# Performance work log

Measured on AMD Instinct MI355X. Metric: run time of the kernel, lower is better.

## Reference

```python
import jax, jax.numpy as jnp
import numpy as np

B, P, CIN = 512, 64, 512       # batch, h*w feature positions, resnet18 channels
HID, EMB, NCLS, T = 512, 512, 96, 30


def setup_inputs() -> dict:
    key = jax.random.key(0)
    ks = jax.random.split(key, 16)
    s = 0.02
    return {
        "features": jax.random.normal(ks[0], (B, P, CIN), jnp.float32),
        "targets": jax.random.randint(ks[1], (B, T), 0, NCLS),
        "max_length": T,
        "Wfc": jax.random.normal(ks[2], (HID, CIN), jnp.float32) * s,
        "bfc": jnp.zeros((HID,), jnp.float32),
        "emb_table": jax.random.normal(ks[3], (NCLS, EMB), jnp.float32) * s,
        "Wa": jax.random.normal(ks[4], (HID, HID + EMB), jnp.float32) * s,
        "ba": jnp.zeros((HID,), jnp.float32),
        "Wc": jax.random.normal(ks[5], (HID, HID + EMB), jnp.float32) * s,
        "bc": jnp.zeros((HID,), jnp.float32),
        "Wih": jax.random.normal(ks[6], (4 * HID, HID), jnp.float32) * s,
        "Whh": jax.random.normal(ks[7], (4 * HID, HID), jnp.float32) * s,
        "bih": jnp.zeros((4 * HID,), jnp.float32),
        "bhh": jnp.zeros((4 * HID,), jnp.float32),
        "Wo": jax.random.normal(ks[8], (NCLS, HID), jnp.float32) * s,
        "bo": jnp.zeros((NCLS,), jnp.float32),
    }


def reference(features, targets, max_length, Wfc, bfc, emb_table, Wa, ba,
              Wc, bc, Wih, Whh, bih, bhh, Wo, bo):
    b = features.shape[0]
    hid = Wfc.shape[0]
    feats = features @ Wfc.T + bfc                       # [b, P, hid]
    # teacher forcing: input at t=0 is token 0, then targets[:, t-1]
    in_ids = jnp.concatenate(
        [jnp.zeros((b, 1), targets.dtype), targets[:, : max_length - 1]], axis=1)
    emb_seq = emb_table[in_ids].transpose(1, 0, 2)       # [T, b, emb]

    def step(carry, emb):
        h, c = carry
        # first softmax is over the hidden dim (as in the original module)
        a = jax.nn.softmax(jnp.concatenate([h, emb], -1) @ Wa.T + ba, axis=-1)  # [b,hid]
        scores = jnp.einsum('bph,bh->bp', feats, a)      # [b, P]
        w = jax.nn.softmax(scores, axis=-1)
        ctx = jnp.einsum('bp,bph->bh', w, feats)         # [b, hid]
        x = jnp.concatenate([emb, ctx], -1) @ Wc.T + bc  # [b, hid]
        gates = x @ Wih.T + bih + h @ Whh.T + bhh        # [b, 4*hid]
        i, f, g, o = jnp.split(gates, 4, axis=-1)        # torch gate order i,f,g,o
        c_new = jax.nn.sigmoid(f) * c + jax.nn.sigmoid(i) * jnp.tanh(g)
        h_new = jax.nn.sigmoid(o) * jnp.tanh(c_new)
        out = h_new @ Wo.T + bo                          # [b, ncls]
        return (h_new, c_new), out

    h0 = jnp.zeros((b, hid), feats.dtype)
    (_, _), outs = jax.lax.scan(step, (h0, h0), emb_seq)
    return outs.transpose(1, 0, 2)                       # [b, T, ncls]
```

## Files before the change

### kernel.cpp

```cpp
#include <hip/hip_runtime.h>
#include <math.h>

static constexpr int BATCH = 512;
static constexpr int PPOS  = 64;
static constexpr int HIDC  = 512;

typedef __attribute__((ext_vector_type(8))) short bf8;
typedef __attribute__((ext_vector_type(4))) float f4;

static __device__ __forceinline__ float sigmoidf_(float x) { return 1.f / (1.f + expf(-x)); }

static __device__ __forceinline__ short f2bf(float x) {
  unsigned u = __float_as_uint(x);
  u = u + 0x7FFF + ((u >> 16) & 1);
  return (short)(u >> 16);
}
static __device__ __forceinline__ float bf2f(short s) {
  return __uint_as_float(((unsigned)(unsigned short)s) << 16);
}

__global__ void transpose_k(const float* __restrict__ src, float* __restrict__ dst, int R, int C, int ld) {
  __shared__ float tile[32][33];
  int c0 = blockIdx.x * 32, r0 = blockIdx.y * 32;
  int x = threadIdx.x;
  for (int yy = threadIdx.y; yy < 32; yy += 8) {
    int r = r0 + yy, c = c0 + x;
    if (r < R && c < C) tile[yy][x] = src[(size_t)r * ld + c];
  }
  __syncthreads();
  for (int yy = threadIdx.y; yy < 32; yy += 8) {
    int c = c0 + yy, r = r0 + x;
    if (r < R && c < C) dst[(size_t)c * R + r] = tile[x][yy];
  }
}

__global__ void bfuse_k(const float* __restrict__ Wih, const float* __restrict__ bc,
                        const float* __restrict__ bih, const float* __restrict__ bhh,
                        float* __restrict__ bf) {
  int n = blockIdx.x * 256 + threadIdx.x;
  float s = bih[n] + bhh[n];
  const float* w = Wih + (size_t)n * 512;
  for (int m = 0; m < 512; m++) s += w[m] * bc[m];
  bf[n] = s;
}

__global__ void build_btg_k(const float* __restrict__ tmp, const float* __restrict__ Whh,
                            short* __restrict__ hi, short* __restrict__ lo) {
  int idx = blockIdx.x * 256 + threadIdx.x;
  int cp = idx >> 10, k = idx & 1023;
  int j = cp >> 2, g = cp & 3;
  int n = g * 512 + j;
  float v = (k < 512) ? tmp[(size_t)(512 + k) * 2048 + n] : Whh[(size_t)n * 512 + (k - 512)];
  short h = f2bf(v);
  hi[idx] = h;
  lo[idx] = f2bf(v - bf2f(h));
}

__global__ void split_k(const float* __restrict__ src, short* __restrict__ hi, short* __restrict__ lo, int n) {
  int i = blockIdx.x * 256 + threadIdx.x;
  if (i < n) {
    float x = src[i];
    short h = f2bf(x);
    hi[i] = h;
    lo[i] = f2bf(x - bf2f(h));
  }
}

__global__ void split_wah_k(const float* __restrict__ Wa, short* __restrict__ hi, short* __restrict__ lo) {
  int idx = blockIdx.x * 256 + threadIdx.x;
  int n = idx >> 9, k = idx & 511;
  float v = Wa[(size_t)n * 1024 + k];
  short h = f2bf(v);
  hi[idx] = h;
  lo[idx] = f2bf(v - bf2f(h));
}

__global__ __launch_bounds__(256) void gemb_k(const float* __restrict__ emb_table, const float* __restrict__ tmp,
                                              const float* __restrict__ bfused, float* __restrict__ Gemb_p) {
  __shared__ float emb_s[4][512];
  int tid = threadIdx.x;
  int n0 = blockIdx.x * 256;
  int e0 = blockIdx.y * 4;
  for (int i = tid; i < 2048; i += 256)
    emb_s[i >> 9][i & 511] = emb_table[(size_t)(e0 + (i >> 9)) * 512 + (i & 511)];
  __syncthreads();
  int n = n0 + tid;
  float acc[4] = {};
  for (int k = 0; k < 512; k++) {
    float w = tmp[(size_t)k * 2048 + n];
#pragma unroll
    for (int e = 0; e < 4; e++) acc[e] += emb_s[e][k] * w;
  }
  int cp = (n & 511) * 4 + (n >> 9);
  float b = bfused[n];
#pragma unroll
  for (int e = 0; e < 4; e++) Gemb_p[(size_t)(e0 + e) * 2048 + cp] = acc[e] + b;
}

__global__ __launch_bounds__(256) void za_k(const float* __restrict__ emb_table, const float* __restrict__ WaT_emb,
                                            const float* __restrict__ ba, float* __restrict__ Za) {
  __shared__ float emb_s[4][512];
  int tid = threadIdx.x;
  int n0 = blockIdx.x * 256;
  int e0 = blockIdx.y * 4;
  for (int i = tid; i < 2048; i += 256)
    emb_s[i >> 9][i & 511] = emb_table[(size_t)(e0 + (i >> 9)) * 512 + (i & 511)];
  __syncthreads();
  int n = n0 + tid;
  float acc[4] = {};
  for (int k = 0; k < 512; k++) {
    float w = WaT_emb[(size_t)k * 512 + n];
#pragma unroll
    for (int e = 0; e < 4; e++) acc[e] += emb_s[e][k] * w;
  }
  float b = ba[n];
#pragma unroll
  for (int e = 0; e < 4; e++) Za[(size_t)(e0 + e) * 512 + n] = acc[e] + b;
}

__global__ __launch_bounds__(256) void feats_mfma_k(const float* __restrict__ A,
                                                    const short* __restrict__ BTh, const short* __restrict__ BTl,
                                                    const float* __restrict__ bias, float* __restrict__ C) {
  __shared__ short Ah[2][64][40], Al[2][64][40], Bh[2][128][40], Bl[2][128][40];
  int blk = blockIdx.x;
  int xt = (blk >> 3) & 3;
  int ytile = (blk >> 5) * 8 + (blk & 7);
  int row0 = ytile * 64, col0 = xt * 128;
  int tid = threadIdx.x;
  int lane = tid & 63, wave = tid >> 6;
  int wm = (wave & 1) * 32, wn = (wave >> 1) * 64;
  int r15 = lane & 15, q8 = (lane >> 4) * 8;
  int smA = tid >> 2, skA = (tid & 3) * 8;
  int smB = tid >> 1, skB = (tid & 1) * 16;
  const float* Ap = A + (size_t)(row0 + smA) * 512 + skA;
  const short* Bhp = BTh + (size_t)(col0 + smB) * 512 + skB;
  const short* Blp = BTl + (size_t)(col0 + smB) * 512 + skB;
  float4 a0 = *(const float4*)Ap, a1 = *(const float4*)(Ap + 4);
  bf8 bh0 = *(const bf8*)Bhp, bh1 = *(const bf8*)(Bhp + 8);
  bf8 bl0 = *(const bf8*)Blp, bl1 = *(const bf8*)(Blp + 8);
  f4 acc[2][4] = {};
  for (int kt = 0; kt < 16; kt++) {
    int buf = kt & 1;
    {
      float av[8] = {a0.x, a0.y, a0.z, a0.w, a1.x, a1.y, a1.z, a1.w};
      bf8 ahv, alv;
#pragma unroll
      for (int i = 0; i < 8; i++) {
        short h = f2bf(av[i]);
        ahv[i] = h;
        alv[i] = f2bf(av[i] - bf2f(h));
      }
      *(bf8*)&Ah[buf][smA][skA] = ahv;
      *(bf8*)&Al[buf][smA][skA] = alv;
      *(bf8*)&Bh[buf][smB][skB] = bh0;
      *(bf8*)&Bh[buf][smB][skB + 8] = bh1;
      *(bf8*)&Bl[buf][smB][skB] = bl0;
      *(bf8*)&Bl[buf][smB][skB + 8] = bl1;
    }
    if (kt + 1 < 16) {
      Ap += 32; Bhp += 32; Blp += 32;
      a0 = *(const float4*)Ap; a1 = *(const float4*)(Ap + 4);
      bh0 = *(const bf8*)Bhp; bh1 = *(const bf8*)(Bhp + 8);
      bl0 = *(const bf8*)Blp; bl1 = *(const bf8*)(Blp + 8);
    }
    __syncthreads();
    bf8 fah[2], fal[2], fbh[4], fbl[4];
#pragma unroll
    for (int r = 0; r < 2; r++) {
      fah[r] = *(const bf8*)&Ah[buf][wm + r * 16 + r15][q8];
      fal[r] = *(const bf8*)&Al[buf][wm + r * 16 + r15][q8];
    }
#pragma unroll
    for (int c = 0; c < 4; c++) {
      fbh[c] = *(const bf8*)&Bh[buf][wn + c * 16 + r15][q8];
      fbl[c] = *(const bf8*)&Bl[buf][wn + c * 16 + r15][q8];
    }
#pragma unroll
    for (int r = 0; r < 2; r++)
#pragma unroll
      for (int c = 0; c < 4; c++) {
        acc[r][c] = __builtin_amdgcn_mfma_f32_16x16x32_bf16(fah[r], fbh[c], acc[r][c], 0, 0, 0);
        acc[r][c] = __builtin_amdgcn_mfma_f32_16x16x32_bf16(fal[r], fbh[c], acc[r][c], 0, 0, 0);
        acc[r][c] = __builtin_amdgcn_mfma_f32_16x16x32_bf16(fah[r], fbl[c], acc[r][c], 0, 0, 0);
      }
  }
#pragma unroll
  for (int r = 0; r < 2; r++)
#pragma unroll
    for (int c = 0; c < 4; c++) {
      int col = col0 + wn + c * 16 + r15;
      float bv = bias[col];
#pragma unroll
      for (int i = 0; i < 4; i++) {
        int row = row0 + wm + r * 16 + (lane >> 4) * 4 + i;
        C[(size_t)row * 512 + col] = acc[r][c][i] + bv;
      }
    }
}

__global__ __launch_bounds__(256) void tmp_mfma_k(const float* __restrict__ A,
                                                  const short* __restrict__ BTh, const short* __restrict__ BTl,
                                                  float* __restrict__ C) {
  __shared__ short Ah[2][64][40], Al[2][64][40], Bh[2][128][40], Bl[2][128][40];
  int row0 = blockIdx.y * 64, col0 = blockIdx.x * 128;
  int tid = threadIdx.x;
  int lane = tid & 63, wave = tid >> 6;
  int wm = (wave & 1) * 32, wn = (wave >> 1) * 64;
  int r15 = lane & 15, q8 = (lane >> 4) * 8;
  int smA = tid >> 2, skA = (tid & 3) * 8;
  int smB = tid >> 1, skB = (tid & 1) * 16;
  const float* Ap = A + (size_t)(row0 + smA) * 512 + skA;
  const short* Bhp = BTh + (size_t)(col0 + smB) * 512 + skB;
  const short* Blp = BTl + (size_t)(col0 + smB) * 512 + skB;
  float4 a0 = *(const float4*)Ap, a1 = *(const float4*)(Ap + 4);
  bf8 bh0 = *(const bf8*)Bhp, bh1 = *(const bf8*)(Bhp + 8);
  bf8 bl0 = *(const bf8*)Blp, bl1 = *(const bf8*)(Blp + 8);
  f4 acc[2][4] = {};
  for (int kt = 0; kt < 16; kt++) {
    int buf = kt & 1;
    {
      float av[8] = {a0.x, a0.y, a0.z, a0.w, a1.x, a1.y, a1.z, a1.w};
      bf8 ahv, alv;
#pragma unroll
      for (int i = 0; i < 8; i++) {
        short h = f2bf(av[i]);
        ahv[i] = h;
        alv[i] = f2bf(av[i] - bf2f(h));
      }
      *(bf8*)&Ah[buf][smA][skA] = ahv;
      *(bf8*)&Al[buf][smA][skA] = alv;
      *(bf8*)&Bh[buf][smB][skB] = bh0;
      *(bf8*)&Bh[buf][smB][skB + 8] = bh1;
      *(bf8*)&Bl[buf][smB][skB] = bl0;
      *(bf8*)&Bl[buf][smB][skB + 8] = bl1;
    }
    if (kt + 1 < 16) {
      Ap += 32; Bhp += 32; Blp += 32;
      a0 = *(const float4*)Ap; a1 = *(const float4*)(Ap + 4);
      bh0 = *(const bf8*)Bhp; bh1 = *(const bf8*)(Bhp + 8);
      bl0 = *(const bf8*)Blp; bl1 = *(const bf8*)(Blp + 8);
    }
    __syncthreads();
    bf8 fah[2], fal[2], fbh[4], fbl[4];
#pragma unroll
    for (int r = 0; r < 2; r++) {
      fah[r] = *(const bf8*)&Ah[buf][wm + r * 16 + r15][q8];
      fal[r] = *(const bf8*)&Al[buf][wm + r * 16 + r15][q8];
    }
#pragma unroll
    for (int c = 0; c < 4; c++) {
      fbh[c] = *(const bf8*)&Bh[buf][wn + c * 16 + r15][q8];
      fbl[c] = *(const bf8*)&Bl[buf][wn + c * 16 + r15][q8];
    }
#pragma unroll
    for (int r = 0; r < 2; r++)
#pragma unroll
      for (int c = 0; c < 4; c++) {
        acc[r][c] = __builtin_amdgcn_mfma_f32_16x16x32_bf16(fah[r], fbh[c], acc[r][c], 0, 0, 0);
        acc[r][c] = __builtin_amdgcn_mfma_f32_16x16x32_bf16(fal[r], fbh[c], acc[r][c], 0, 0, 0);
        acc[r][c] = __builtin_amdgcn_mfma_f32_16x16x32_bf16(fah[r], fbl[c], acc[r][c], 0, 0, 0);
      }
  }
#pragma unroll
  for (int r = 0; r < 2; r++)
#pragma unroll
    for (int c = 0; c < 4; c++) {
      int col = col0 + wn + c * 16 + r15;
#pragma unroll
      for (int i = 0; i < 4; i++) {
        int row = row0 + wm + r * 16 + (lane >> 4) * 4 + i;
        C[(size_t)row * 2048 + col] = acc[r][c][i];
      }
    }
}

__global__ __launch_bounds__(256) void z_mfma_k(const short* __restrict__ h_hi, const short* __restrict__ h_lo,
                                                const short* __restrict__ BTh, const short* __restrict__ BTl,
                                                float* __restrict__ zbuf) {
  __shared__ short Ah[2][32][72], Al[2][32][72], Bh[2][32][72], Bl[2][32][72];
  int tid = threadIdx.x;
  int lane = tid & 63, wave = tid >> 6;
  int wm = (wave & 1) * 16, wn = (wave >> 1) * 16;
  int r15 = lane & 15, q4 = (lane >> 4) * 4, q8 = (lane >> 4) * 8;
  int row0 = blockIdx.y * 32, col0 = blockIdx.x * 32;
  int kz = blockIdx.z * 256;
  int sm = tid >> 3, sk = (tid & 7) * 8;
  const short* ahp = h_hi + (size_t)(row0 + sm) * 512 + kz + sk;
  const short* alp = h_lo + (size_t)(row0 + sm) * 512 + kz + sk;
  const short* bhp = BTh + (size_t)(col0 + sm) * 512 + kz + sk;
  const short* blp = BTl + (size_t)(col0 + sm) * 512 + kz + sk;
  bf8 ah = *(const bf8*)ahp, al = *(const bf8*)alp;
  bf8 bh = *(const bf8*)bhp, bl = *(const bf8*)blp;
  f4 acc = {};
  for (int kt = 0; kt < 4; kt++) {
    int buf = kt & 1;
    *(bf8*)&Ah[buf][sm][sk] = ah;
    *(bf8*)&Al[buf][sm][sk] = al;
    *(bf8*)&Bh[buf][sm][sk] = bh;
    *(bf8*)&Bl[buf][sm][sk] = bl;
    if (kt + 1 < 4) {
      ahp += 64; alp += 64; bhp += 64; blp += 64;
      ah = *(const bf8*)ahp; al = *(const bf8*)alp;
      bh = *(const bf8*)bhp; bl = *(const bf8*)blp;
    }
    __syncthreads();
#pragma unroll
    for (int ks = 0; ks < 2; ks++) {
      bf8 fah = *(const bf8*)&Ah[buf][wm + r15][ks * 32 + q8];
      bf8 fal = *(const bf8*)&Al[buf][wm + r15][ks * 32 + q8];
      bf8 fbh = *(const bf8*)&Bh[buf][wn + r15][ks * 32 + q8];
      bf8 fbl = *(const bf8*)&Bl[buf][wn + r15][ks * 32 + q8];
      acc = __builtin_amdgcn_mfma_f32_16x16x32_bf16(fah, fbh, acc, 0, 0, 0);
      acc = __builtin_amdgcn_mfma_f32_16x16x32_bf16(fal, fbh, acc, 0, 0, 0);
      acc = __builtin_amdgcn_mfma_f32_16x16x32_bf16(fah, fbl, acc, 0, 0, 0);
    }
  }
  float* zo = zbuf + (size_t)blockIdx.z * (512 * 512);
  int col = col0 + wn + r15;
#pragma unroll
  for (int i = 0; i < 4; i++)
    zo[(size_t)(row0 + wm + q4 + i) * 512 + col] = acc[i];
}

__global__ __launch_bounds__(512) void attn_fin_k(const float* __restrict__ zbuf,
                                                  const int* __restrict__ targets, int t, int T,
                                                  const float* __restrict__ Za, const float* __restrict__ feats,
                                                  short* __restrict__ ctx_hi, short* __restrict__ ctx_lo) {
  __shared__ float a_s[512];
  __shared__ float redm[8], reds[8];
  __shared__ float sc_s[64];
  __shared__ float w_s[64];
  __shared__ float cpart[8][512];
  int tid = threadIdx.x;
  int wid = tid >> 6, lane = tid & 63;
  int b = blockIdx.x;
  int id = (t == 0) ? 0 : targets[b * T + t - 1];

  const float4* fbase = (const float4*)(feats + (size_t)b * PPOS * 512);
  float4 f1[8], f2[8];
#pragma unroll
  for (int q = 0; q < 8; q++) {
    int p = wid * 8 + q;
    f1[q] = fbase[(size_t)p * 128 + lane];
    f2[q] = fbase[(size_t)p * 128 + 64 + lane];
  }

  float zv = zbuf[(size_t)b * 512 + tid] + zbuf[(size_t)(512 * 512) + b * 512 + tid]
           + Za[(size_t)id * 512 + tid];
  float m = zv;
#pragma unroll
  for (int off = 32; off; off >>= 1) m = fmaxf(m, __shfl_xor(m, off, 64));
  if (lane == 0) redm[wid] = m;
  __syncthreads();
  float M = redm[0];
#pragma unroll
  for (int w = 1; w < 8; w++) M = fmaxf(M, redm[w]);
  float e = expf(zv - M);
  float s = e;
#pragma unroll
  for (int off = 32; off; off >>= 1) s += __shfl_xor(s, off, 64);
  if (lane == 0) reds[wid] = s;
  __syncthreads();
  float S = 0.f;
#pragma unroll
  for (int w = 0; w < 8; w++) S += reds[w];
  a_s[tid] = e * (1.f / S);
  __syncthreads();

  float4 a1 = ((const float4*)a_s)[lane];
  float4 a2 = ((const float4*)a_s)[lane + 64];
#pragma unroll
  for (int q = 0; q < 8; q++) {
    float d = f1[q].x * a1.x + f1[q].y * a1.y + f1[q].z * a1.z + f1[q].w * a1.w
            + f2[q].x * a2.x + f2[q].y * a2.y + f2[q].z * a2.z + f2[q].w * a2.w;
#pragma unroll
    for (int off = 32; off; off >>= 1) d += __shfl_xor(d, off, 64);
    if (lane == 0) sc_s[wid * 8 + q] = d;
  }
  __syncthreads();

  if (wid == 0) {
    float v = sc_s[lane];
    float mm = v;
#pragma unroll
    for (int off = 32; off; off >>= 1) mm = fmaxf(mm, __shfl_xor(mm, off, 64));
    float ee = expf(v - mm);
    float ss = ee;
#pragma unroll
    for (int off = 32; off; off >>= 1) ss += __shfl_xor(ss, off, 64);
    w_s[lane] = ee / ss;
  }
  __syncthreads();

  float4 c1 = {0.f, 0.f, 0.f, 0.f}, c2 = {0.f, 0.f, 0.f, 0.f};
#pragma unroll
  for (int q = 0; q < 8; q++) {
    float wp = w_s[wid * 8 + q];
    c1.x += wp * f1[q].x; c1.y += wp * f1[q].y; c1.z += wp * f1[q].z; c1.w += wp * f1[q].w;
    c2.x += wp * f2[q].x; c2.y += wp * f2[q].y; c2.z += wp * f2[q].z; c2.w += wp * f2[q].w;
  }
  ((float4*)&cpart[wid][0])[lane] = c1;
  ((float4*)&cpart[wid][256])[lane] = c2;
  __syncthreads();

  float acc = 0.f;
#pragma unroll
  for (int w = 0; w < 8; w++) acc += cpart[w][tid];
  short hh = f2bf(acc);
  ctx_hi[(size_t)b * 512 + tid] = hh;
  ctx_lo[(size_t)b * 512 + tid] = f2bf(acc - bf2f(hh));
}

__global__ __launch_bounds__(256) void gates_mfma_k(const short* __restrict__ ctx_hi, const short* __restrict__ ctx_lo,
                                                    const short* __restrict__ h_hi_in, const short* __restrict__ h_lo_in,
                                                    const int* __restrict__ targets, int t, int T,
                                                    const short* __restrict__ BTh, const short* __restrict__ BTl,
                                                    const float* __restrict__ Gemb_p,
                                                    float* __restrict__ cbuf, float* __restrict__ h_new,
                                                    short* __restrict__ h_hi_out, short* __restrict__ h_lo_out) {
  __shared__ short Ah[2][32][72], Al[2][32][72], Bh[2][64][72], Bl[2][64][72];
  __shared__ float Cs[32][68];
  int tid = threadIdx.x;
  int lane = tid & 63, wave = tid >> 6;
  int wn = wave * 16;
  int r15 = lane & 15, q8 = (lane >> 4) * 8;
  int row0 = blockIdx.y * 32, col0 = blockIdx.x * 64;
  int smA = tid >> 3, skA = (tid & 7) * 8;
  int smB = tid >> 2, skB = (tid & 3) * 16;
  const short* actx_h = ctx_hi + (size_t)(row0 + smA) * 512;
  const short* actx_l = ctx_lo + (size_t)(row0 + smA) * 512;
  const short* ahst_h = h_hi_in + (size_t)(row0 + smA) * 512;
  const short* ahst_l = h_lo_in + (size_t)(row0 + smA) * 512;
  const short* Bhp = BTh + (size_t)(col0 + smB) * 1024 + skB;
  const short* Blp = BTl + (size_t)(col0 + smB) * 1024 + skB;
  bf8 ah = *(const bf8*)(actx_h + skA), al = *(const bf8*)(actx_l + skA);
  bf8 bh0 = *(const bf8*)Bhp, bh1 = *(const bf8*)(Bhp + 8);
  bf8 bl0 = *(const bf8*)Blp, bl1 = *(const bf8*)(Blp + 8);
  f4 acc[2] = {};
  for (int kt = 0; kt < 16; kt++) {
    int buf = kt & 1;
    *(bf8*)&Ah[buf][smA][skA] = ah;
    *(bf8*)&Al[buf][smA][skA] = al;
    *(bf8*)&Bh[buf][smB][skB] = bh0;
    *(bf8*)&Bh[buf][smB][skB + 8] = bh1;
    *(bf8*)&Bl[buf][smB][skB] = bl0;
    *(bf8*)&Bl[buf][smB][skB + 8] = bl1;
    if (kt + 1 < 16) {
      int kk = (kt + 1) * 64 + skA;
      if (kk < 512) {
        ah = *(const bf8*)(actx_h + kk);
        al = *(const bf8*)(actx_l + kk);
      } else {
        ah = *(const bf8*)(ahst_h + kk - 512);
        al = *(const bf8*)(ahst_l + kk - 512);
      }
      Bhp += 64; Blp += 64;
      bh0 = *(const bf8*)Bhp; bh1 = *(const bf8*)(Bhp + 8);
      bl0 = *(const bf8*)Blp; bl1 = *(const bf8*)(Blp + 8);
    }
    __syncthreads();
#pragma unroll
    for (int ks = 0; ks < 2; ks++) {
      bf8 fah[2], fal[2];
#pragma unroll
      for (int r = 0; r < 2; r++) {
        fah[r] = *(const bf8*)&Ah[buf][r * 16 + r15][ks * 32 + q8];
        fal[r] = *(const bf8*)&Al[buf][r * 16 + r15][ks * 32 + q8];
      }
      bf8 fbh = *(const bf8*)&Bh[buf][wn + r15][ks * 32 + q8];
      bf8 fbl = *(const bf8*)&Bl[buf][wn + r15][ks * 32 + q8];
#pragma unroll
      for (int r = 0; r < 2; r++) {
        acc[r] = __builtin_amdgcn_mfma_f32_16x16x32_bf16(fah[r], fbh, acc[r], 0, 0, 0);
        acc[r] = __builtin_amdgcn_mfma_f32_16x16x32_bf16(fal[r], fbh, acc[r], 0, 0, 0);
        acc[r] = __builtin_amdgcn_mfma_f32_16x16x32_bf16(fah[r], fbl, acc[r], 0, 0, 0);
      }
    }
  }
#pragma unroll
  for (int r = 0; r < 2; r++)
#pragma unroll
    for (int i = 0; i < 4; i++)
      Cs[r * 16 + (lane >> 4) * 4 + i][wn + r15] = acc[r][i];
  __syncthreads();
#pragma unroll
  for (int it = 0; it < 2; it++) {
    int idx = it * 256 + tid;
    int row = idx >> 4, jj = idx & 15;
    int b = row0 + row;
    int jg = (col0 >> 2) + jj;
    int id = (t == 0) ? 0 : targets[b * T + t - 1];
    float4 g4 = *(const float4*)(Gemb_p + (size_t)id * 2048 + col0 + jj * 4);
    float ig = sigmoidf_(Cs[row][jj * 4 + 0] + g4.x);
    float fg = sigmoidf_(Cs[row][jj * 4 + 1] + g4.y);
    float gg = tanhf(Cs[row][jj * 4 + 2] + g4.z);
    float og = sigmoidf_(Cs[row][jj * 4 + 3] + g4.w);
    float cn = fg * cbuf[(size_t)b * 512 + jg] + ig * gg;
    float hn = og * tanhf(cn);
    cbuf[(size_t)b * 512 + jg] = cn;
    h_new[(size_t)b * 512 + jg] = hn;
    short hh = f2bf(hn);
    h_hi_out[(size_t)b * 512 + jg] = hh;
    h_lo_out[(size_t)b * 512 + jg] = f2bf(hn - bf2f(hh));
  }
}

__global__ __launch_bounds__(256) void out_gemm_k(const float* __restrict__ h_hist, const float* __restrict__ WoT,
                                                  const float* __restrict__ bo, float* __restrict__ out, int T) {
  __shared__ float As[16][68];
  __shared__ float Bs[16][96];
  int tid = threadIdx.x;
  int tx = tid & 15, ty = tid >> 4;
  int row0 = blockIdx.x * 64;
  float acc[4][6] = {};
  for (int k0 = 0; k0 < 512; k0 += 16) {
    {
      int r = tid >> 2;
      int kk = (tid & 3) * 4;
      float4 v = *(const float4*)(h_hist + (size_t)(row0 + r) * 512 + k0 + kk);
      As[kk + 0][r] = v.x; As[kk + 1][r] = v.y; As[kk + 2][r] = v.z; As[kk + 3][r] = v.w;
    }
#pragma unroll
    for (int i = 0; i < 6; i++) {
      int e = tid + 256 * i;
      int kb = e / 96, n = e - kb * 96;
      Bs[kb][n] = WoT[(size_t)(k0 + kb) * 96 + n];
    }
    __syncthreads();
#pragma unroll
    for (int q = 0; q < 16; q++) {
      float av[4], bvv[6];
#pragma unroll
      for (int i = 0; i < 4; i++) av[i] = As[q][ty * 4 + i];
#pragma unroll
      for (int j = 0; j < 6; j++) bvv[j] = Bs[q][tx * 6 + j];
#pragma unroll
      for (int i = 0; i < 4; i++)
#pragma unroll
        for (int j = 0; j < 6; j++) acc[i][j] += av[i] * bvv[j];
    }
    __syncthreads();
  }
#pragma unroll
  for (int i = 0; i < 4; i++)
#pragma unroll
    for (int j = 0; j < 6; j++) {
      int row = row0 + ty * 4 + i;
      int tt = row >> 9, bb = row & 511;
      int cc = tx * 6 + j;
      out[((size_t)bb * T + tt) * 96 + cc] = acc[i][j] + bo[cc];
    }
}

extern "C" void kernel_launch(void* const* d_in, const int* in_sizes, int n_in,
                              void* d_out, int out_size, void* d_ws, size_t ws_size,
                              hipStream_t stream) {
  const float* features  = (const float*)d_in[0];
  const int*   targets   = (const int*)d_in[1];
  const float* Wfc       = (const float*)d_in[3];
  const float* bfc       = (const float*)d_in[4];
  const float* emb_table = (const float*)d_in[5];
  const float* Wa        = (const float*)d_in[6];
  const float* ba        = (const float*)d_in[7];
  const float* Wc        = (const float*)d_in[8];
  const float* bc        = (const float*)d_in[9];
  const float* Wih       = (const float*)d_in[10];
  const float* Whh       = (const float*)d_in[11];
  const float* bih       = (const float*)d_in[12];
  const float* bhh       = (const float*)d_in[13];
  const float* Wo        = (const float*)d_in[14];
  const float* bo        = (const float*)d_in[15];
  float* out = (float*)d_out;
  int T = in_sizes[1] / BATCH;

  char* base = (char*)d_ws;
  auto alloc = [&](size_t bytes) -> char* {
    char* p = base;
    base += (bytes + 255) & ~(size_t)255;
    return p;
  };
  float* feats   = (float*)alloc((size_t)BATCH * PPOS * HIDC * 4);
  float* WaT_emb = (float*)alloc(512 * 512 * 4);
  float* WcT     = (float*)alloc(1024 * 512 * 4);
  float* tmp     = (float*)alloc((size_t)1024 * 2048 * 4);
  short* Wih_hi  = (short*)alloc((size_t)2048 * 512 * 2);
  short* Wih_lo  = (short*)alloc((size_t)2048 * 512 * 2);
  short* BTg_hi  = (short*)alloc((size_t)2048 * 1024 * 2);
  short* BTg_lo  = (short*)alloc((size_t)2048 * 1024 * 2);
  short* Wfc_hi  = (short*)alloc(512 * 512 * 2);
  short* Wfc_lo  = (short*)alloc(512 * 512 * 2);
  short* WaH_hi  = (short*)alloc(512 * 512 * 2);
  short* WaH_lo  = (short*)alloc(512 * 512 * 2);
  float* Gemb_p  = (float*)alloc(96 * 2048 * 4);
  float* Za      = (float*)alloc(96 * 512 * 4);
  float* bfused  = (float*)alloc(2048 * 4);
  float* WoT     = (float*)alloc(512 * 96 * 4);
  float* cbuf    = (float*)alloc(BATCH * HIDC * 4);
  float* zbuf    = (float*)alloc((size_t)2 * BATCH * HIDC * 4);
  short* ctx_hi  = (short*)alloc(BATCH * HIDC * 2);
  short* ctx_lo  = (short*)alloc(BATCH * HIDC * 2);
  short* h_hi    = (short*)alloc(BATCH * HIDC * 2);
  short* h_lo    = (short*)alloc(BATCH * HIDC * 2);
  float* h_hist  = (float*)alloc((size_t)T * BATCH * HIDC * 4);

  dim3 tb(32, 8);
  transpose_k<<<dim3(16, 16), tb, 0, stream>>>(Wa + 512, WaT_emb, 512, 512, 1024);
  transpose_k<<<dim3(32, 16), tb, 0, stream>>>(Wc, WcT, 512, 1024, 1024);
  transpose_k<<<dim3(16, 3),  tb, 0, stream>>>(Wo, WoT, 96, 512, 512);

  split_k<<<(2048 * 512) / 256, 256, 0, stream>>>(Wih, Wih_hi, Wih_lo, 2048 * 512);
  split_k<<<(512 * 512) / 256, 256, 0, stream>>>(Wfc, Wfc_hi, Wfc_lo, 512 * 512);
  split_wah_k<<<(512 * 512) / 256, 256, 0, stream>>>(Wa, WaH_hi, WaH_lo);

  tmp_mfma_k<<<dim3(16, 16), 256, 0, stream>>>(WcT, Wih_hi, Wih_lo, tmp);

  bfuse_k<<<8, 256, 0, stream>>>(Wih, bc, bih, bhh, bfused);
  build_btg_k<<<(2048 * 1024) / 256, 256, 0, stream>>>(tmp, Whh, BTg_hi, BTg_lo);
  gemb_k<<<dim3(8, 24), 256, 0, stream>>>(emb_table, tmp, bfused, Gemb_p);
  za_k<<<dim3(2, 24), 256, 0, stream>>>(emb_table, WaT_emb, ba, Za);

  feats_mfma_k<<<2048, 256, 0, stream>>>(features, Wfc_hi, Wfc_lo, bfc, feats);

  hipMemsetAsync(cbuf, 0, (size_t)BATCH * HIDC * 4, stream);
  hipMemsetAsync(h_hi, 0, (size_t)BATCH * HIDC * 2, stream);
  hipMemsetAsync(h_lo, 0, (size_t)BATCH * HIDC * 2, stream);

  for (int t = 0; t < T; t++) {
    float* h_new = h_hist + (size_t)t * BATCH * HIDC;
    z_mfma_k<<<dim3(16, 16, 2), 256, 0, stream>>>(h_hi, h_lo, WaH_hi, WaH_lo, zbuf);
    attn_fin_k<<<512, 512, 0, stream>>>(zbuf, targets, t, T, Za, feats, ctx_hi, ctx_lo);
    gates_mfma_k<<<dim3(32, 16), 256, 0, stream>>>(ctx_hi, ctx_lo, h_hi, h_lo, targets, t, T,
                                                   BTg_hi, BTg_lo, Gemb_p, cbuf, h_new, h_hi, h_lo);
  }
  out_gemm_k<<<(T * BATCH) / 64, 256, 0, stream>>>(h_hist, WoT, bo, out, T);
}
```

Measured before the change: 1.445 ms.

## Pre-pack weight operands in MFMA fragment order and load B directly to registers

```diff
diff --git a/kernel.cpp b/kernel.cpp
--- a/kernel.cpp
+++ b/kernel.cpp
@@ -44,18 +44,6 @@
   bf[n] = s;
 }
 
-__global__ void build_btg_k(const float* __restrict__ tmp, const float* __restrict__ Whh,
-                            short* __restrict__ hi, short* __restrict__ lo) {
-  int idx = blockIdx.x * 256 + threadIdx.x;
-  int cp = idx >> 10, k = idx & 1023;
-  int j = cp >> 2, g = cp & 3;
-  int n = g * 512 + j;
-  float v = (k < 512) ? tmp[(size_t)(512 + k) * 2048 + n] : Whh[(size_t)n * 512 + (k - 512)];
-  short h = f2bf(v);
-  hi[idx] = h;
-  lo[idx] = f2bf(v - bf2f(h));
-}
-
 __global__ void split_k(const float* __restrict__ src, short* __restrict__ hi, short* __restrict__ lo, int n) {
   int i = blockIdx.x * 256 + threadIdx.x;
   if (i < n) {
@@ -66,10 +54,27 @@
   }
 }
 
-__global__ void split_wah_k(const float* __restrict__ Wa, short* __restrict__ hi, short* __restrict__ lo) {
+__global__ void pack_split_k(const float* __restrict__ src, int ld,
+                             short* __restrict__ hi, short* __restrict__ lo) {
   int idx = blockIdx.x * 256 + threadIdx.x;
-  int n = idx >> 9, k = idx & 511;
-  float v = Wa[(size_t)n * 1024 + k];
+  int j = idx & 7, lane = (idx >> 3) & 63, kf = (idx >> 9) & 15, cg = idx >> 13;
+  int n = cg * 16 + (lane & 15);
+  int k = kf * 32 + ((lane >> 4) << 3) + j;
+  float v = src[(size_t)n * ld + k];
+  short h = f2bf(v);
+  hi[idx] = h;
+  lo[idx] = f2bf(v - bf2f(h));
+}
+
+__global__ void build_btg_pack_k(const float* __restrict__ tmp, const float* __restrict__ Whh,
+                                 short* __restrict__ hi, short* __restrict__ lo) {
+  int idx = blockIdx.x * 256 + threadIdx.x;
+  int j = idx & 7, lane = (idx >> 3) & 63, kf = (idx >> 9) & 31, cg = idx >> 14;
+  int cp = cg * 16 + (lane & 15);
+  int k = kf * 32 + ((lane >> 4) << 3) + j;
+  int jj = cp >> 2, g = cp & 3;
+  int n = g * 512 + jj;
+  float v = (k < 512) ? tmp[(size_t)(512 + k) * 2048 + n] : Whh[(size_t)n * 512 + (k - 512)];
   short h = f2bf(v);
   hi[idx] = h;
   lo[idx] = f2bf(v - bf2f(h));
@@ -119,13 +124,91 @@
 }
 
 __global__ __launch_bounds__(256) void feats_mfma_k(const float* __restrict__ A,
-                                                    const short* __restrict__ BTh, const short* __restrict__ BTl,
+                                                    const short* __restrict__ Ph, const short* __restrict__ Pl,
                                                     const float* __restrict__ bias, float* __restrict__ C) {
-  __shared__ short Ah[2][64][40], Al[2][64][40], Bh[2][128][40], Bl[2][128][40];
+  __shared__ short Ah[2][64][40], Al[2][64][40];
   int blk = blockIdx.x;
   int xt = (blk >> 3) & 3;
   int ytile = (blk >> 5) * 8 + (blk & 7);
   int row0 = ytile * 64, col0 = xt * 128;
+  int tid = threadIdx.x;
+  int lane = tid & 63, wave = tid >> 6;
+  int wm = (wave & 1) * 32, wn = (wave >> 1) * 64;
+  int r15 = lane & 15, q8 = (lane >> 4) * 8;
+  int smA = tid >> 2, skA = (tid & 3) * 8;
+  const float* Ap = A + (size_t)(row0 + smA) * 512 + skA;
+  int cg0 = (col0 + wn) >> 4;
+  const short* pbh = Ph + (size_t)cg0 * 8192 + lane * 8;
+  const short* pbl = Pl + (size_t)cg0 * 8192 + lane * 8;
+  float4 a0 = *(const float4*)Ap, a1 = *(const float4*)(Ap + 4);
+  bf8 bhc[4], blc[4], bhn[4], bln[4];
+#pragma unroll
+  for (int c = 0; c < 4; c++) {
+    bhc[c] = *(const bf8*)(pbh + c * 8192);
+    blc[c] = *(const bf8*)(pbl + c * 8192);
+  }
+  f4 acc[2][4] = {};
+#pragma unroll 2
+  for (int kt = 0; kt < 16; kt++) {
+    int buf = kt & 1;
+    {
+      float av[8] = {a0.x, a0.y, a0.z, a0.w, a1.x, a1.y, a1.z, a1.w};
+      bf8 ahv, alv;
+#pragma unroll
+      for (int i = 0; i < 8; i++) {
+        short h = f2bf(av[i]);
+        ahv[i] = h;
+        alv[i] = f2bf(av[i] - bf2f(h));
+      }
+      *(bf8*)&Ah[buf][smA][skA] = ahv;
+      *(bf8*)&Al[buf][smA][skA] = alv;
+    }
+    if (kt + 1 < 16) {
+      Ap += 32;
+      a0 = *(const float4*)Ap; a1 = *(const float4*)(Ap + 4);
+#pragma unroll
+      for (int c = 0; c < 4; c++) {
+        bhn[c] = *(const bf8*)(pbh + c * 8192 + (kt + 1) * 512);
+        bln[c] = *(const bf8*)(pbl + c * 8192 + (kt + 1) * 512);
+      }
+    }
+    __syncthreads();
+    bf8 fah[2], fal[2];
+#pragma unroll
+    for (int r = 0; r < 2; r++) {
+      fah[r] = *(const bf8*)&Ah[buf][wm + r * 16 + r15][q8];
+      fal[r] = *(const bf8*)&Al[buf][wm + r * 16 + r15][q8];
+    }
+#pragma unroll
+    for (int r = 0; r < 2; r++)
+#pragma unroll
+      for (int c = 0; c < 4; c++) {
+        acc[r][c] = __builtin_amdgcn_mfma_f32_16x16x32_bf16(fah[r], bhc[c], acc[r][c], 0, 0, 0);
+        acc[r][c] = __builtin_amdgcn_mfma_f32_16x16x32_bf16(fal[r], bhc[c], acc[r][c], 0, 0, 0);
+        acc[r][c] = __builtin_amdgcn_mfma_f32_16x16x32_bf16(fah[r], blc[c], acc[r][c], 0, 0, 0);
+      }
+#pragma unroll
+    for (int c = 0; c < 4; c++) { bhc[c] = bhn[c]; blc[c] = bln[c]; }
+  }
+#pragma unroll
+  for (int r = 0; r < 2; r++)
+#pragma unroll
+    for (int c = 0; c < 4; c++) {
+      int col = col0 + wn + c * 16 + r15;
+      float bv = bias[col];
+#pragma unroll
+      for (int i = 0; i < 4; i++) {
+        int row = row0 + wm + r * 16 + (lane >> 4) * 4 + i;
+        C[(size_t)row * 512 + col] = acc[r][c][i] + bv;
+      }
+    }
+}
+
+__global__ __launch_bounds__(256) void tmp_mfma_k(const float* __restrict__ A,
+                                                  const short* __restrict__ BTh, const short* __restrict__ BTl,
+                                                  float* __restrict__ C) {
+  __shared__ short Ah[2][64][40], Al[2][64][40], Bh[2][128][40], Bl[2][128][40];
+  int row0 = blockIdx.y * 64, col0 = blockIdx.x * 128;
   int tid = threadIdx.x;
   int lane = tid & 63, wave = tid >> 6;
   int wm = (wave & 1) * 32, wn = (wave >> 1) * 64;
@@ -189,83 +272,6 @@
 #pragma unroll
     for (int c = 0; c < 4; c++) {
       int col = col0 + wn + c * 16 + r15;
-      float bv = bias[col];
-#pragma unroll
-      for (int i = 0; i < 4; i++) {
-        int row = row0 + wm + r * 16 + (lane >> 4) * 4 + i;
-        C[(size_t)row * 512 + col] = acc[r][c][i] + bv;
-      }
-    }
-}
-
-__global__ __launch_bounds__(256) void tmp_mfma_k(const float* __restrict__ A,
-                                                  const short* __restrict__ BTh, const short* __restrict__ BTl,
-                                                  float* __restrict__ C) {
-  __shared__ short Ah[2][64][40], Al[2][64][40], Bh[2][128][40], Bl[2][128][40];
-  int row0 = blockIdx.y * 64, col0 = blockIdx.x * 128;
-  int tid = threadIdx.x;
-  int lane = tid & 63, wave = tid >> 6;
-  int wm = (wave & 1) * 32, wn = (wave >> 1) * 64;
-  int r15 = lane & 15, q8 = (lane >> 4) * 8;
-  int smA = tid >> 2, skA = (tid & 3) * 8;
-  int smB = tid >> 1, skB = (tid & 1) * 16;
-  const float* Ap = A + (size_t)(row0 + smA) * 512 + skA;
-  const short* Bhp = BTh + (size_t)(col0 + smB) * 512 + skB;
-  const short* Blp = BTl + (size_t)(col0 + smB) * 512 + skB;
-  float4 a0 = *(const float4*)Ap, a1 = *(const float4*)(Ap + 4);
-  bf8 bh0 = *(const bf8*)Bhp, bh1 = *(const bf8*)(Bhp + 8);
-  bf8 bl0 = *(const bf8*)Blp, bl1 = *(const bf8*)(Blp + 8);
-  f4 acc[2][4] = {};
-  for (int kt = 0; kt < 16; kt++) {
-    int buf = kt & 1;
-    {
-      float av[8] = {a0.x, a0.y, a0.z, a0.w, a1.x, a1.y, a1.z, a1.w};
-      bf8 ahv, alv;
-#pragma unroll
-      for (int i = 0; i < 8; i++) {
-        short h = f2bf(av[i]);
-        ahv[i] = h;
-        alv[i] = f2bf(av[i] - bf2f(h));
-      }
-      *(bf8*)&Ah[buf][smA][skA] = ahv;
-      *(bf8*)&Al[buf][smA][skA] = alv;
-      *(bf8*)&Bh[buf][smB][skB] = bh0;
-      *(bf8*)&Bh[buf][smB][skB + 8] = bh1;
-      *(bf8*)&Bl[buf][smB][skB] = bl0;
-      *(bf8*)&Bl[buf][smB][skB + 8] = bl1;
-    }
-    if (kt + 1 < 16) {
-      Ap += 32; Bhp += 32; Blp += 32;
-      a0 = *(const float4*)Ap; a1 = *(const float4*)(Ap + 4);
-      bh0 = *(const bf8*)Bhp; bh1 = *(const bf8*)(Bhp + 8);
-      bl0 = *(const bf8*)Blp; bl1 = *(const bf8*)(Blp + 8);
-    }
-    __syncthreads();
-    bf8 fah[2], fal[2], fbh[4], fbl[4];
-#pragma unroll
-    for (int r = 0; r < 2; r++) {
-      fah[r] = *(const bf8*)&Ah[buf][wm + r * 16 + r15][q8];
-      fal[r] = *(const bf8*)&Al[buf][wm + r * 16 + r15][q8];
-    }
-#pragma unroll
-    for (int c = 0; c < 4; c++) {
-      fbh[c] = *(const bf8*)&Bh[buf][wn + c * 16 + r15][q8];
-      fbl[c] = *(const bf8*)&Bl[buf][wn + c * 16 + r15][q8];
-    }
-#pragma unroll
-    for (int r = 0; r < 2; r++)
-#pragma unroll
-      for (int c = 0; c < 4; c++) {
-        acc[r][c] = __builtin_amdgcn_mfma_f32_16x16x32_bf16(fah[r], fbh[c], acc[r][c], 0, 0, 0);
-        acc[r][c] = __builtin_amdgcn_mfma_f32_16x16x32_bf16(fal[r], fbh[c], acc[r][c], 0, 0, 0);
-        acc[r][c] = __builtin_amdgcn_mfma_f32_16x16x32_bf16(fah[r], fbl[c], acc[r][c], 0, 0, 0);
-      }
-  }
-#pragma unroll
-  for (int r = 0; r < 2; r++)
-#pragma unroll
-    for (int c = 0; c < 4; c++) {
-      int col = col0 + wn + c * 16 + r15;
 #pragma unroll
       for (int i = 0; i < 4; i++) {
         int row = row0 + wm + r * 16 + (lane >> 4) * 4 + i;
@@ -275,9 +281,9 @@
 }
 
 __global__ __launch_bounds__(256) void z_mfma_k(const short* __restrict__ h_hi, const short* __restrict__ h_lo,
-                                                const short* __restrict__ BTh, const short* __restrict__ BTl,
+                                                const short* __restrict__ Ph, const short* __restrict__ Pl,
                                                 float* __restrict__ zbuf) {
-  __shared__ short Ah[2][32][72], Al[2][32][72], Bh[2][32][72], Bl[2][32][72];
+  __shared__ short Ah[2][32][72], Al[2][32][72];
   int tid = threadIdx.x;
   int lane = tid & 63, wave = tid >> 6;
   int wm = (wave & 1) * 16, wn = (wave >> 1) * 16;
@@ -287,33 +293,42 @@
   int sm = tid >> 3, sk = (tid & 7) * 8;
   const short* ahp = h_hi + (size_t)(row0 + sm) * 512 + kz + sk;
   const short* alp = h_lo + (size_t)(row0 + sm) * 512 + kz + sk;
-  const short* bhp = BTh + (size_t)(col0 + sm) * 512 + kz + sk;
-  const short* blp = BTl + (size_t)(col0 + sm) * 512 + kz + sk;
+  int cg = (col0 + wn) >> 4;
+  const short* pbh = Ph + (size_t)cg * 8192 + (size_t)blockIdx.z * 8 * 512 + lane * 8;
+  const short* pbl = Pl + (size_t)cg * 8192 + (size_t)blockIdx.z * 8 * 512 + lane * 8;
   bf8 ah = *(const bf8*)ahp, al = *(const bf8*)alp;
-  bf8 bh = *(const bf8*)bhp, bl = *(const bf8*)blp;
+  bf8 bhc[2], blc[2], bhn[2], bln[2];
+#pragma unroll
+  for (int ks = 0; ks < 2; ks++) {
+    bhc[ks] = *(const bf8*)(pbh + ks * 512);
+    blc[ks] = *(const bf8*)(pbl + ks * 512);
+  }
   f4 acc = {};
+#pragma unroll 2
   for (int kt = 0; kt < 4; kt++) {
     int buf = kt & 1;
     *(bf8*)&Ah[buf][sm][sk] = ah;
     *(bf8*)&Al[buf][sm][sk] = al;
-    *(bf8*)&Bh[buf][sm][sk] = bh;
-    *(bf8*)&Bl[buf][sm][sk] = bl;
     if (kt + 1 < 4) {
-      ahp += 64; alp += 64; bhp += 64; blp += 64;
+      ahp += 64; alp += 64;
       ah = *(const bf8*)ahp; al = *(const bf8*)alp;
-      bh = *(const bf8*)bhp; bl = *(const bf8*)blp;
+#pragma unroll
+      for (int ks = 0; ks < 2; ks++) {
+        bhn[ks] = *(const bf8*)(pbh + ((kt + 1) * 2 + ks) * 512);
+        bln[ks] = *(const bf8*)(pbl + ((kt + 1) * 2 + ks) * 512);
+      }
     }
     __syncthreads();
 #pragma unroll
     for (int ks = 0; ks < 2; ks++) {
       bf8 fah = *(const bf8*)&Ah[buf][wm + r15][ks * 32 + q8];
       bf8 fal = *(const bf8*)&Al[buf][wm + r15][ks * 32 + q8];
-      bf8 fbh = *(const bf8*)&Bh[buf][wn + r15][ks * 32 + q8];
-      bf8 fbl = *(const bf8*)&Bl[buf][wn + r15][ks * 32 + q8];
-      acc = __builtin_amdgcn_mfma_f32_16x16x32_bf16(fah, fbh, acc, 0, 0, 0);
-      acc = __builtin_amdgcn_mfma_f32_16x16x32_bf16(fal, fbh, acc, 0, 0, 0);
-      acc = __builtin_amdgcn_mfma_f32_16x16x32_bf16(fah, fbl, acc, 0, 0, 0);
-    }
+      acc = __builtin_amdgcn_mfma_f32_16x16x32_bf16(fah, bhc[ks], acc, 0, 0, 0);
+      acc = __builtin_amdgcn_mfma_f32_16x16x32_bf16(fal, bhc[ks], acc, 0, 0, 0);
+      acc = __builtin_amdgcn_mfma_f32_16x16x32_bf16(fah, blc[ks], acc, 0, 0, 0);
+    }
+#pragma unroll
+    for (int ks = 0; ks < 2; ks++) { bhc[ks] = bhn[ks]; blc[ks] = bln[ks]; }
   }
   float* zo = zbuf + (size_t)blockIdx.z * (512 * 512);
   int col = col0 + wn + r15;
@@ -414,11 +429,11 @@
 __global__ __launch_bounds__(256) void gates_mfma_k(const short* __restrict__ ctx_hi, const short* __restrict__ ctx_lo,
                                                     const short* __restrict__ h_hi_in, const short* __restrict__ h_lo_in,
                                                     const int* __restrict__ targets, int t, int T,
-                                                    const short* __restrict__ BTh, const short* __restrict__ BTl,
+                                                    const short* __restrict__ Ph, const short* __restrict__ Pl,
                                                     const float* __restrict__ Gemb_p,
                                                     float* __restrict__ cbuf, float* __restrict__ h_new,
                                                     short* __restrict__ h_hi_out, short* __restrict__ h_lo_out) {
-  __shared__ short Ah[2][32][72], Al[2][32][72], Bh[2][64][72], Bl[2][64][72];
+  __shared__ short Ah[2][32][72], Al[2][32][72];
   __shared__ float Cs[32][68];
   int tid = threadIdx.x;
   int lane = tid & 63, wave = tid >> 6;
@@ -426,25 +441,26 @@
   int r15 = lane & 15, q8 = (lane >> 4) * 8;
   int row0 = blockIdx.y * 32, col0 = blockIdx.x * 64;
   int smA = tid >> 3, skA = (tid & 7) * 8;
-  int smB = tid >> 2, skB = (tid & 3) * 16;
   const short* actx_h = ctx_hi + (size_t)(row0 + smA) * 512;
   const short* actx_l = ctx_lo + (size_t)(row0 + smA) * 512;
   const short* ahst_h = h_hi_in + (size_t)(row0 + smA) * 512;
   const short* ahst_l = h_lo_in + (size_t)(row0 + smA) * 512;
-  const short* Bhp = BTh + (size_t)(col0 + smB) * 1024 + skB;
-  const short* Blp = BTl + (size_t)(col0 + smB) * 1024 + skB;
+  int cg = (col0 >> 4) + wave;
+  const short* pbh = Ph + (size_t)cg * 16384 + lane * 8;
+  const short* pbl = Pl + (size_t)cg * 16384 + lane * 8;
   bf8 ah = *(const bf8*)(actx_h + skA), al = *(const bf8*)(actx_l + skA);
-  bf8 bh0 = *(const bf8*)Bhp, bh1 = *(const bf8*)(Bhp + 8);
-  bf8 bl0 = *(const bf8*)Blp, bl1 = *(const bf8*)(Blp + 8);
+  bf8 bhc[2], blc[2], bhn[2], bln[2];
+#pragma unroll
+  for (int ks = 0; ks < 2; ks++) {
+    bhc[ks] = *(const bf8*)(pbh + ks * 512);
+    blc[ks] = *(const bf8*)(pbl + ks * 512);
+  }
   f4 acc[2] = {};
+#pragma unroll 2
   for (int kt = 0; kt < 16; kt++) {
     int buf = kt & 1;
     *(bf8*)&Ah[buf][smA][skA] = ah;
     *(bf8*)&Al[buf][smA][skA] = al;
-    *(bf8*)&Bh[buf][smB][skB] = bh0;
-    *(bf8*)&Bh[buf][smB][skB + 8] = bh1;
-    *(bf8*)&Bl[buf][smB][skB] = bl0;
-    *(bf8*)&Bl[buf][smB][skB + 8] = bl1;
     if (kt + 1 < 16) {
       int kk = (kt + 1) * 64 + skA;
       if (kk < 512) {
@@ -454,9 +470,11 @@
         ah = *(const bf8*)(ahst_h + kk - 512);
         al = *(const bf8*)(ahst_l + kk - 512);
       }
-      Bhp += 64; Blp += 64;
-      bh0 = *(const bf8*)Bhp; bh1 = *(const bf8*)(Bhp + 8);
-      bl0 = *(const bf8*)Blp; bl1 = *(const bf8*)(Blp + 8);
+#pragma unroll
+      for (int ks = 0; ks < 2; ks++) {
+        bhn[ks] = *(const bf8*)(pbh + ((kt + 1) * 2 + ks) * 512);
+        bln[ks] = *(const bf8*)(pbl + ((kt + 1) * 2 + ks) * 512);
+      }
     }
     __syncthreads();
 #pragma unroll
@@ -467,15 +485,15 @@
         fah[r] = *(const bf8*)&Ah[buf][r * 16 + r15][ks * 32 + q8];
         fal[r] = *(const bf8*)&Al[buf][r * 16 + r15][ks * 32 + q8];
       }
-      bf8 fbh = *(const bf8*)&Bh[buf][wn + r15][ks * 32 + q8];
-      bf8 fbl = *(const bf8*)&Bl[buf][wn + r15][ks * 32 + q8];
 #pragma unroll
       for (int r = 0; r < 2; r++) {
-        acc[r] = __builtin_amdgcn_mfma_f32_16x16x32_bf16(fah[r], fbh, acc[r], 0, 0, 0);
-        acc[r] = __builtin_amdgcn_mfma_f32_16x16x32_bf16(fal[r], fbh, acc[r], 0, 0, 0);
-        acc[r] = __builtin_amdgcn_mfma_f32_16x16x32_bf16(fah[r], fbl, acc[r], 0, 0, 0);
-      }
-    }
+        acc[r] = __builtin_amdgcn_mfma_f32_16x16x32_bf16(fah[r], bhc[ks], acc[r], 0, 0, 0);
+        acc[r] = __builtin_amdgcn_mfma_f32_16x16x32_bf16(fal[r], bhc[ks], acc[r], 0, 0, 0);
+        acc[r] = __builtin_amdgcn_mfma_f32_16x16x32_bf16(fah[r], blc[ks], acc[r], 0, 0, 0);
+      }
+    }
+#pragma unroll
+    for (int ks = 0; ks < 2; ks++) { bhc[ks] = bhn[ks]; blc[ks] = bln[ks]; }
   }
 #pragma unroll
   for (int r = 0; r < 2; r++)
@@ -585,12 +603,12 @@
   float* tmp     = (float*)alloc((size_t)1024 * 2048 * 4);
   short* Wih_hi  = (short*)alloc((size_t)2048 * 512 * 2);
   short* Wih_lo  = (short*)alloc((size_t)2048 * 512 * 2);
-  short* BTg_hi  = (short*)alloc((size_t)2048 * 1024 * 2);
-  short* BTg_lo  = (short*)alloc((size_t)2048 * 1024 * 2);
-  short* Wfc_hi  = (short*)alloc(512 * 512 * 2);
-  short* Wfc_lo  = (short*)alloc(512 * 512 * 2);
-  short* WaH_hi  = (short*)alloc(512 * 512 * 2);
-  short* WaH_lo  = (short*)alloc(512 * 512 * 2);
+  short* PBTg_hi = (short*)alloc((size_t)2048 * 1024 * 2);
+  short* PBTg_lo = (short*)alloc((size_t)2048 * 1024 * 2);
+  short* Pfc_hi  = (short*)alloc(512 * 512 * 2);
+  short* Pfc_lo  = (short*)alloc(512 * 512 * 2);
+  short* Pwa_hi  = (short*)alloc(512 * 512 * 2);
+  short* Pwa_lo  = (short*)alloc(512 * 512 * 2);
   float* Gemb_p  = (float*)alloc(96 * 2048 * 4);
   float* Za      = (float*)alloc(96 * 512 * 4);
   float* bfused  = (float*)alloc(2048 * 4);
@@ -609,17 +627,17 @@
   transpose_k<<<dim3(16, 3),  tb, 0, stream>>>(Wo, WoT, 96, 512, 512);
 
   split_k<<<(2048 * 512) / 256, 256, 0, stream>>>(Wih, Wih_hi, Wih_lo, 2048 * 512);
-  split_k<<<(512 * 512) / 256, 256, 0, stream>>>(Wfc, Wfc_hi, Wfc_lo, 512 * 512);
-  split_wah_k<<<(512 * 512) / 256, 256, 0, stream>>>(Wa, WaH_hi, WaH_lo);
+  pack_split_k<<<(512 * 512) / 256, 256, 0, stream>>>(Wfc, 512, Pfc_hi, Pfc_lo);
+  pack_split_k<<<(512 * 512) / 256, 256, 0, stream>>>(Wa, 1024, Pwa_hi, Pwa_lo);
 
   tmp_mfma_k<<<dim3(16, 16), 256, 0, stream>>>(WcT, Wih_hi, Wih_lo, tmp);
 
   bfuse_k<<<8, 256, 0, stream>>>(Wih, bc, bih, bhh, bfused);
-  build_btg_k<<<(2048 * 1024) / 256, 256, 0, stream>>>(tmp, Whh, BTg_hi, BTg_lo);
+  build_btg_pack_k<<<(2048 * 1024) / 256, 256, 0, stream>>>(tmp, Whh, PBTg_hi, PBTg_lo);
   gemb_k<<<dim3(8, 24), 256, 0, stream>>>(emb_table, tmp, bfused, Gemb_p);
   za_k<<<dim3(2, 24), 256, 0, stream>>>(emb_table, WaT_emb, ba, Za);
 
-  feats_mfma_k<<<2048, 256, 0, stream>>>(features, Wfc_hi, Wfc_lo, bfc, feats);
+  feats_mfma_k<<<2048, 256, 0, stream>>>(features, Pfc_hi, Pfc_lo, bfc, feats);
 
   hipMemsetAsync(cbuf, 0, (size_t)BATCH * HIDC * 4, stream);
   hipMemsetAsync(h_hi, 0, (size_t)BATCH * HIDC * 2, stream);
@@ -627,10 +645,10 @@
 
   for (int t = 0; t < T; t++) {
     float* h_new = h_hist + (size_t)t * BATCH * HIDC;
-    z_mfma_k<<<dim3(16, 16, 2), 256, 0, stream>>>(h_hi, h_lo, WaH_hi, WaH_lo, zbuf);
+    z_mfma_k<<<dim3(16, 16, 2), 256, 0, stream>>>(h_hi, h_lo, Pwa_hi, Pwa_lo, zbuf);
     attn_fin_k<<<512, 512, 0, stream>>>(zbuf, targets, t, T, Za, feats, ctx_hi, ctx_lo);
     gates_mfma_k<<<dim3(32, 16), 256, 0, stream>>>(ctx_hi, ctx_lo, h_hi, h_lo, targets, t, T,
-                                                   BTg_hi, BTg_lo, Gemb_p, cbuf, h_new, h_hi, h_lo);
+                                                   PBTg_hi, PBTg_lo, Gemb_p, cbuf, h_new, h_hi, h_lo);
   }
   out_gemm_k<<<(T * BATCH) / 64, 256, 0, stream>>>(h_hist, WoT, bo, out, T);
 }
```

Result: faster. 1.335 ms (-7.6%).
